# Performance work log

Measured on AMD Instinct MI355X. Metric: run time of the kernel, lower is better.

Reference implementation:

```python
import jax, jax.numpy as jnp
import numpy as np

B, E, WIN, DX, DZ, RAW = 2048, 32, 10, 14, 14, 22

def _leaky(x):
    return jnp.where(x >= 0, x, 0.01 * x)

def setup_inputs():
    key = jax.random.key(0)
    ks = jax.random.split(key, 20)
    def w(k, i, o):
        return jax.random.normal(k, (i, o), dtype=jnp.float32) / np.float32(np.sqrt(i))
    def b(k, o):
        return jax.random.normal(k, (o,), dtype=jnp.float32) * 0.01
    return {
        "raw_obs": jax.random.normal(ks[0], (B, WIN, 1, RAW), dtype=jnp.float32),
        "state_prev": jax.random.normal(ks[1], (B, E, WIN, DX), dtype=jnp.float32),
        "pm_w1": w(ks[2], WIN * DX, 256), "pm_b1": b(ks[3], 256),
        "pm_w3": w(ks[4], 256, 512), "pm_b3": b(ks[5], 512),
        "pm_wm2": w(ks[6], 512, DX), "pm_bm2": b(ks[7], DX),
        "sm_w2": w(ks[8], WIN * RAW, 256), "sm_b2": b(ks[9], 256),
        "sm_w3": w(ks[10], 256, 256), "sm_b3": b(ks[11], 256),
        "sm_w5": w(ks[12], 256, 64), "sm_b5": b(ks[13], 64),
        "sm_w6": w(ks[14], 64, DZ), "sm_b6": b(ks[15], DZ),
        "on_w1": w(ks[16], DZ, 32), "on_b1": b(ks[17], 32),
        "on_w2": w(ks[18], 32, DZ), "on_b2": b(ks[19], DZ),
    }

def reference(raw_obs, state_prev, pm_w1, pm_b1, pm_w3, pm_b3, pm_wm2, pm_bm2,
              sm_w2, sm_b2, sm_w3, sm_b3, sm_w5, sm_b5, sm_w6, sm_b6,
              on_w1, on_b1, on_w2, on_b2):
    bs, ens, win, dx = state_prev.shape
    dz = sm_w6.shape[1]
    # --- process model (LinearFlipout evaluated at mean weights) ---
    x = state_prev.reshape(bs * ens, win * dx)
    x = _leaky(x @ pm_w1 + pm_b1)
    x = _leaky(x @ pm_w3 + pm_b3)
    state_pred = (x @ pm_wm2 + pm_bm2).reshape(bs, ens, dx)   # [B,E,dx]
    state_m = state_pred.mean(axis=1)                          # [B,dx]
    A = state_pred - state_m[:, None, :]                       # [B,E,dx]
    # --- sensor model: torch repeat(E,1,1,1) tiles ensemble-major, the final
    # reshape reinterprets as batch-major; replicate that layout faithfully ---
    s = jnp.tile(raw_obs, (ens, 1, 1, 1)).reshape(bs * ens, win * raw_obs.shape[-1])
    s = _leaky(s @ sm_w2 + sm_b2)
    s = _leaky(s @ sm_w3 + sm_b3)
    s = _leaky(s @ sm_w5 + sm_b5)
    s = s @ sm_w6 + sm_b6
    ensemble_z = s.reshape(bs, ens, dz)                        # [B,E,dz]
    z = ensemble_z.mean(axis=1, keepdims=True)                 # [B,1,dz]
    # --- observation noise R = diag_embed(square(mlp(z)+c) + init) ---
    r = jax.nn.relu(z @ on_w1 + on_b1) @ on_w2 + on_b2
    r = jnp.square(r + 0.001) + 0.038729833
    R = r.reshape(bs, dz)[:, :, None] * jnp.eye(dz, dtype=r.dtype)  # [B,dz,dz]
    # --- EnKF correction ---
    S = jnp.einsum('bei,bej->bij', A, A)                       # AT @ A, [B,dx,dx]
    innovation = S / (ens - 1) + R
    K = (S / (ens - 1)) @ jnp.linalg.inv(innovation)           # [B,dx,dz]
    diff = ensemble_z - state_pred                             # (y - H_XT)^T, [B,E,dz]
    gain = jnp.einsum('bij,bej->bei', K, diff)                 # [B,E,dx]
    state_corrected = state_pred + gain
    return (state_corrected,
            state_corrected.mean(axis=1, keepdims=True),
            state_m[:, None, :],
            z,
            ensemble_z)
```

## Files before the change

kernel.cpp:

```cpp
#include <hip/hip_runtime.h>

typedef unsigned short u16;
typedef __attribute__((ext_vector_type(8))) short short8;
typedef __attribute__((ext_vector_type(4))) float floatx4;

#define MFMA_BF16 __builtin_amdgcn_mfma_f32_16x16x32_bf16

__device__ __forceinline__ u16 f2bf(float f) {
    union { float f; unsigned int i; } v; v.f = f;
    unsigned int u = v.i;
    u += 0x7fffu + ((u >> 16) & 1u);
    return (u16)(u >> 16);
}
__device__ __forceinline__ float leaky(float x) { return x >= 0.f ? x : 0.01f * x; }

#define H1S 264
#define RS 232
#define H3S 72
#define CS 136

#define O1 917504
#define O2 946176
#define O3 974848
#define O4 1003520

#define PW1   0
#define PW3   40960
#define PWM2  172032
#define PSW2  180224
#define PSW3  237568
#define PSW5  303104
#define PSW6  319488
#define PTOTAL 320512
#define WS_NEEDED 641024
#define WS_BIG (641024 + 3670016)

struct PackSeg { const float* W; int K, N, S, base, count; };
struct PackArgs { PackSeg seg[7]; };

__global__ __launch_bounds__(256) void pack_all(PackArgs pa, u16* __restrict__ P) {
    int u = blockIdx.x * 256 + threadIdx.x;
    if (u >= PTOTAL) return;
#pragma unroll
    for (int i = 0; i < 7; i++) {
        if (u >= pa.seg[i].base && u < pa.seg[i].base + pa.seg[i].count) {
            int v = u - pa.seg[i].base;
            int j = v & 7;
            int l = (v >> 3) & 63;
            int ts = v >> 9;
            int s = ts % pa.seg[i].S;
            int t = ts / pa.seg[i].S;
            int k = s * 32 + (l >> 4) * 8 + j;
            int n = t * 16 + (l & 15);
            P[u] = (k < pa.seg[i].K && n < pa.seg[i].N)
                       ? f2bf(pa.seg[i].W[k * pa.seg[i].N + n]) : (u16)0;
            return;
        }
    }
}

__device__ __forceinline__ short8 load_x_frag(const float* __restrict__ X,
                                              int row, int s, int q) {
    const float* p = X + row * 140;
    float4 v0 = {0.f, 0.f, 0.f, 0.f}, v1 = {0.f, 0.f, 0.f, 0.f};
    int col0 = s * 32 + q * 8;
    if (s < 4) {
        v0 = *(const float4*)(p + col0);
        v1 = *(const float4*)(p + col0 + 4);
    } else {
        if (q <= 1) v0 = *(const float4*)(p + col0);
        if (q == 0) v1 = *(const float4*)(p + col0 + 4);
    }
    short8 r;
    r[0] = (short)f2bf(v0.x); r[1] = (short)f2bf(v0.y);
    r[2] = (short)f2bf(v0.z); r[3] = (short)f2bf(v0.w);
    r[4] = (short)f2bf(v1.x); r[5] = (short)f2bf(v1.y);
    r[6] = (short)f2bf(v1.z); r[7] = (short)f2bf(v1.w);
    return r;
}

__global__ __launch_bounds__(256) void merged_mlp(
    const float* __restrict__ Rg, const float* __restrict__ Xg,
    const u16* __restrict__ Pk,
    const float* __restrict__ b1, const float* __restrict__ b3,
    const float* __restrict__ bm2,
    const float* __restrict__ b2, const float* __restrict__ sb3,
    const float* __restrict__ b5, const float* __restrict__ b6,
    float* __restrict__ ez_out,
    float* __restrict__ sp_ws)
{
    __shared__ __align__(16) u16 ldsH[64 * H1S];
    __shared__ __align__(16) u16 ldsC[64 * CS];

    const int tid  = threadIdx.x;
    const int lane = tid & 63;
    const int wave = tid >> 6;
    const int q    = lane >> 4;
    const int n16  = lane & 15;

    if (blockIdx.x < 64) {
        const u16* w2p = Pk + PSW2;
        const u16* w3p = Pk + PSW3;
        const u16* w5p = Pk + PSW5;
        const u16* w6p = Pk + PSW6;
        const int row0 = blockIdx.x * 32;

        for (int idx = tid; idx < 32 * 56; idx += 256) {
            int r = idx / 56, c4 = idx - r * 56;
            float4 v = {0.f, 0.f, 0.f, 0.f};
            if (c4 < 55) v = *(const float4*)&Rg[(row0 + r) * 220 + c4 * 4];
            u16* dst = &ldsH[r * RS + c4 * 4];
            dst[0] = f2bf(v.x); dst[1] = f2bf(v.y); dst[2] = f2bf(v.z); dst[3] = f2bf(v.w);
        }
        __syncthreads();

        {
            floatx4 zero = {0.f, 0.f, 0.f, 0.f};
            floatx4 acc[2][4];
            for (int rt = 0; rt < 2; rt++)
                for (int ct = 0; ct < 4; ct++) acc[rt][ct] = zero;
#pragma unroll
            for (int s = 0; s < 7; s++) {
                short8 a0 = *(const short8*)&ldsH[n16 * RS + s * 32 + q * 8];
                short8 a1 = *(const short8*)&ldsH[(n16 + 16) * RS + s * 32 + q * 8];
#pragma unroll
                for (int ct = 0; ct < 4; ct++) {
                    int t = wave * 4 + ct;
                    short8 bf = *(const short8*)&w2p[((t * 7 + s) * 64 + lane) * 8];
                    acc[0][ct] = MFMA_BF16(a0, bf, acc[0][ct], 0, 0, 0);
                    acc[1][ct] = MFMA_BF16(a1, bf, acc[1][ct], 0, 0, 0);
                }
            }
#pragma unroll
            for (int ct = 0; ct < 4; ct++) {
                int col = (wave * 4 + ct) * 16 + n16;
                float bias = b2[col];
#pragma unroll
                for (int rt = 0; rt < 2; rt++)
#pragma unroll
                    for (int r = 0; r < 4; r++)
                        ldsC[(rt * 16 + q * 4 + r) * H1S + col] = f2bf(leaky(acc[rt][ct][r] + bias));
            }
        }
        __syncthreads();

        {
            floatx4 zero = {0.f, 0.f, 0.f, 0.f};
            floatx4 acc[2][4];
            for (int rt = 0; rt < 2; rt++)
                for (int ct = 0; ct < 4; ct++) acc[rt][ct] = zero;
#pragma unroll
            for (int s = 0; s < 8; s++) {
                short8 a0 = *(const short8*)&ldsC[n16 * H1S + s * 32 + q * 8];
                short8 a1 = *(const short8*)&ldsC[(n16 + 16) * H1S + s * 32 + q * 8];
#pragma unroll
                for (int ct = 0; ct < 4; ct++) {
                    int t = wave * 4 + ct;
                    short8 bf = *(const short8*)&w3p[((t * 8 + s) * 64 + lane) * 8];
                    acc[0][ct] = MFMA_BF16(a0, bf, acc[0][ct], 0, 0, 0);
                    acc[1][ct] = MFMA_BF16(a1, bf, acc[1][ct], 0, 0, 0);
                }
            }
#pragma unroll
            for (int ct = 0; ct < 4; ct++) {
                int col = (wave * 4 + ct) * 16 + n16;
                float bias = sb3[col];
#pragma unroll
                for (int rt = 0; rt < 2; rt++)
#pragma unroll
                    for (int r = 0; r < 4; r++)
                        ldsH[(rt * 16 + q * 4 + r) * H1S + col] = f2bf(leaky(acc[rt][ct][r] + bias));
            }
        }
        __syncthreads();

        {
            floatx4 zero = {0.f, 0.f, 0.f, 0.f};
            floatx4 acc[2] = {zero, zero};
#pragma unroll
            for (int s = 0; s < 8; s++) {
                short8 a0 = *(const short8*)&ldsH[n16 * H1S + s * 32 + q * 8];
                short8 a1 = *(const short8*)&ldsH[(n16 + 16) * H1S + s * 32 + q * 8];
                short8 bf = *(const short8*)&w5p[((wave * 8 + s) * 64 + lane) * 8];
                acc[0] = MFMA_BF16(a0, bf, acc[0], 0, 0, 0);
                acc[1] = MFMA_BF16(a1, bf, acc[1], 0, 0, 0);
            }
            int col = wave * 16 + n16;
            float bias = b5[col];
#pragma unroll
            for (int rt = 0; rt < 2; rt++)
#pragma unroll
                for (int r = 0; r < 4; r++)
                    ldsC[(rt * 16 + q * 4 + r) * H3S + col] = f2bf(leaky(acc[rt][r] + bias));
        }
        __syncthreads();

        if (wave < 2) {
            floatx4 zero = {0.f, 0.f, 0.f, 0.f};
            floatx4 acc[2] = {zero, zero};
            int s = wave;
            short8 a0 = *(const short8*)&ldsC[n16 * H3S + s * 32 + q * 8];
            short8 a1 = *(const short8*)&ldsC[(n16 + 16) * H3S + s * 32 + q * 8];
            short8 bf = *(const short8*)&w6p[(s * 64 + lane) * 8];
            acc[0] = MFMA_BF16(a0, bf, acc[0], 0, 0, 0);
            acc[1] = MFMA_BF16(a1, bf, acc[1], 0, 0, 0);
            float* pacc = (float*)ldsH;
#pragma unroll
            for (int rt = 0; rt < 2; rt++)
#pragma unroll
                for (int r = 0; r < 4; r++)
                    pacc[(wave * 32 + rt * 16 + q * 4 + r) * 16 + n16] = acc[rt][r];
        }
        __syncthreads();
        {
            const float* pacc = (const float*)ldsH;
            for (int idx = tid; idx < 512; idx += 256) {
                int r = idx >> 4, c = idx & 15;
                float v = pacc[idx] + pacc[512 + idx];
                if (c < 14) ez_out[(row0 + r) * 14 + c] = v + b6[c];
            }
        }
    } else {
        const u16* w1p  = Pk + PW1;
        const u16* w3p  = Pk + PW3;
        const u16* wm2p = Pk + PWM2;
        const int bb   = blockIdx.x - 64;
        const int row0 = bb * 64;

        {
            floatx4 zero = {0.f, 0.f, 0.f, 0.f};
            floatx4 acc[4][4];
            for (int rt = 0; rt < 4; rt++)
                for (int ct = 0; ct < 4; ct++) acc[rt][ct] = zero;
#pragma unroll
            for (int s = 0; s < 5; s++) {
                short8 a[4];
#pragma unroll
                for (int rt = 0; rt < 4; rt++)
                    a[rt] = load_x_frag(Xg, row0 + rt * 16 + n16, s, q);
#pragma unroll
                for (int ct = 0; ct < 4; ct++) {
                    int t = wave * 4 + ct;
                    short8 bf = *(const short8*)&w1p[((t * 5 + s) * 64 + lane) * 8];
#pragma unroll
                    for (int rt = 0; rt < 4; rt++)
                        acc[rt][ct] = MFMA_BF16(a[rt], bf, acc[rt][ct], 0, 0, 0);
                }
            }
#pragma unroll
            for (int ct = 0; ct < 4; ct++) {
                int col = (wave * 4 + ct) * 16 + n16;
                float bias = b1[col];
#pragma unroll
                for (int rt = 0; rt < 4; rt++)
#pragma unroll
                    for (int r = 0; r < 4; r++)
                        ldsH[(rt * 16 + q * 4 + r) * H1S + col] = f2bf(leaky(acc[rt][ct][r] + bias));
            }
        }
        __syncthreads();

        floatx4 acc3[4];
        {
            floatx4 zero = {0.f, 0.f, 0.f, 0.f};
            for (int rt = 0; rt < 4; rt++) acc3[rt] = zero;
        }
#pragma unroll
        for (int c = 0; c < 4; c++) {
            {
                floatx4 zero = {0.f, 0.f, 0.f, 0.f};
                floatx4 acc[4][2];
                for (int rt = 0; rt < 4; rt++)
                    for (int ct = 0; ct < 2; ct++) acc[rt][ct] = zero;
#pragma unroll
                for (int s = 0; s < 8; s++) {
                    short8 a[4];
#pragma unroll
                    for (int rt = 0; rt < 4; rt++)
                        a[rt] = *(const short8*)&ldsH[(rt * 16 + n16) * H1S + s * 32 + q * 8];
#pragma unroll
                    for (int ct = 0; ct < 2; ct++) {
                        int tg = c * 8 + wave * 2 + ct;
                        short8 bf = *(const short8*)&w3p[((tg * 8 + s) * 64 + lane) * 8];
#pragma unroll
                        for (int rt = 0; rt < 4; rt++)
                            acc[rt][ct] = MFMA_BF16(a[rt], bf, acc[rt][ct], 0, 0, 0);
                    }
                }
#pragma unroll
                for (int ct = 0; ct < 2; ct++) {
                    int cl = (wave * 2 + ct) * 16 + n16;
                    float bias = b3[c * 128 + cl];
#pragma unroll
                    for (int rt = 0; rt < 4; rt++)
#pragma unroll
                        for (int r = 0; r < 4; r++)
                            ldsC[(rt * 16 + q * 4 + r) * CS + cl] = f2bf(leaky(acc[rt][ct][r] + bias));
                }
            }
            __syncthreads();
            {
                int sg = c * 4 + wave;
                short8 bf = *(const short8*)&wm2p[(sg * 64 + lane) * 8];
#pragma unroll
                for (int rt = 0; rt < 4; rt++) {
                    short8 a = *(const short8*)&ldsC[(rt * 16 + n16) * CS + wave * 32 + q * 8];
                    acc3[rt] = MFMA_BF16(a, bf, acc3[rt], 0, 0, 0);
                }
            }
            __syncthreads();
        }

        {
            float* pacc = (float*)ldsH;
#pragma unroll
            for (int rt = 0; rt < 4; rt++)
#pragma unroll
                for (int r = 0; r < 4; r++)
                    pacc[(wave * 64 + rt * 16 + q * 4 + r) * 16 + n16] = acc3[rt][r];
        }
        __syncthreads();
        {
            const float* pacc = (const float*)ldsH;
            for (int idx = tid; idx < 1024; idx += 256) {
                int r = idx >> 4, c = idx & 15;
                float v = pacc[idx] + pacc[1024 + idx] + pacc[2048 + idx] + pacc[3072 + idx];
                if (c < 14) sp_ws[(row0 + r) * 14 + c] = v + bm2[c];
            }
        }
    }
}

__global__ __launch_bounds__(64) void enkf_tail(
    const float* __restrict__ sp_all,
    const float* __restrict__ on_w1, const float* __restrict__ on_b1,
    const float* __restrict__ on_w2, const float* __restrict__ on_b2,
    float* out)
{
    __shared__ float spv[32][14];
    __shared__ float ezv[32][14];
    __shared__ float smv[14], zzv[14], rrv[14];
    __shared__ float M[14][14], Kmat[14][14];
    __shared__ float G[14][28];
    __shared__ float fac[14];
    __shared__ float hbuf[32];

    const int l = threadIdx.x;
    const int b = blockIdx.x;

    for (int idx = l; idx < 448; idx += 64) ((float*)spv)[idx] = sp_all[b * 448 + idx];
    {
        const float* ezsrc = out + O4 + (b & 63) * 448;
        for (int idx = l; idx < 448; idx += 64) ((float*)ezv)[idx] = ezsrc[idx];
    }

    if (l < 14) {
        float s1 = 0.f, s2 = 0.f;
        for (int e = 0; e < 32; e++) { s1 += spv[e][l]; s2 += ezv[e][l]; }
        smv[l] = s1 * (1.f / 32.f);
        zzv[l] = s2 * (1.f / 32.f);
    }
    if (l < 32) {
        float t = on_b1[l];
        for (int k = 0; k < 14; k++) t += zzv[k] * on_w1[k * 32 + l];
        hbuf[l] = t > 0.f ? t : 0.f;
    }
    if (l < 14) {
        float t = on_b2[l];
        for (int k = 0; k < 32; k++) t += hbuf[k] * on_w2[k * 14 + l];
        t += 0.001f;
        rrv[l] = t * t + 0.038729833f;
    }
    for (int idx = l; idx < 196; idx += 64) {
        int i = idx / 14, j = idx - i * 14;
        float s = 0.f;
        for (int e = 0; e < 32; e++) s += (spv[e][i] - smv[i]) * (spv[e][j] - smv[j]);
        s *= (1.f / 31.f);
        M[i][j] = s;
        G[i][j] = s + (i == j ? rrv[i] : 0.f);
        G[i][14 + j] = (i == j) ? 1.f : 0.f;
    }
    for (int c = 0; c < 14; c++) {
        float pinv = 1.f / G[c][c];
        if (l < 28) G[c][l] *= pinv;
        if (l < 14 && l != c) fac[l] = G[l][c];
        for (int idx = l; idx < 392; idx += 64) {
            int i = idx / 28, j = idx - i * 28;
            if (i != c) G[i][j] -= fac[i] * G[c][j];
        }
    }
    for (int idx = l; idx < 196; idx += 64) {
        int i = idx / 14, j = idx - i * 14;
        float s = 0.f;
        for (int k = 0; k < 14; k++) s += M[i][k] * G[k][14 + j];
        Kmat[i][j] = s;
    }
    for (int idx = l; idx < 448; idx += 64) {
        int e = idx / 14, i = idx - e * 14;
        float g = 0.f;
        for (int j = 0; j < 14; j++) g += Kmat[i][j] * (ezv[e][j] - spv[e][j]);
        out[b * 448 + idx] = spv[e][i] + g;
        out[O4 + b * 448 + idx] = ezv[e][i];
    }
    if (l < 14) {
        float g = 0.f;
        for (int j = 0; j < 14; j++) g += Kmat[l][j] * (zzv[j] - smv[j]);
        out[O1 + b * 14 + l] = smv[l] + g;
        out[O2 + b * 14 + l] = smv[l];
        out[O3 + b * 14 + l] = zzv[l];
    }
}

extern "C" void kernel_launch(void* const* d_in, const int* in_sizes, int n_in,
                              void* d_out, int out_size, void* d_ws, size_t ws_size,
                              hipStream_t stream) {
    (void)in_sizes; (void)n_in; (void)out_size; (void)ws_size;

    const float* raw_obs    = (const float*)d_in[0];
    const float* state_prev = (const float*)d_in[1];
    const float* pm_w1  = (const float*)d_in[2];
    const float* pm_b1  = (const float*)d_in[3];
    const float* pm_w3  = (const float*)d_in[4];
    const float* pm_b3  = (const float*)d_in[5];
    const float* pm_wm2 = (const float*)d_in[6];
    const float* pm_bm2 = (const float*)d_in[7];
    const float* sm_w2  = (const float*)d_in[8];
    const float* sm_b2  = (const float*)d_in[9];
    const float* sm_w3  = (const float*)d_in[10];
    const float* sm_b3  = (const float*)d_in[11];
    const float* sm_w5  = (const float*)d_in[12];
    const float* sm_b5  = (const float*)d_in[13];
    const float* sm_w6  = (const float*)d_in[14];
    const float* sm_b6  = (const float*)d_in[15];
    const float* on_w1  = (const float*)d_in[16];
    const float* on_b1  = (const float*)d_in[17];
    const float* on_w2  = (const float*)d_in[18];
    const float* on_b2  = (const float*)d_in[19];

    float* out = (float*)d_out;
    u16* P = (u16*)d_ws;
    float* sp_ws = (float*)((char*)d_ws + WS_NEEDED);

    PackArgs pa;
    pa.seg[0] = { pm_w1,  140, 256, 5,  PW1,  40960  };
    pa.seg[1] = { pm_w3,  256, 512, 8,  PW3,  131072 };
    pa.seg[2] = { pm_wm2, 512, 14,  16, PWM2, 8192   };
    pa.seg[3] = { sm_w2,  220, 256, 7,  PSW2, 57344  };
    pa.seg[4] = { sm_w3,  256, 256, 8,  PSW3, 65536  };
    pa.seg[5] = { sm_w5,  256, 64,  8,  PSW5, 16384  };
    pa.seg[6] = { sm_w6,  64,  14,  2,  PSW6, 1024   };
    pack_all<<<(PTOTAL + 255) / 256, 256, 0, stream>>>(pa, P);

    merged_mlp<<<1088, 256, 0, stream>>>(raw_obs, state_prev, P,
                                         pm_b1, pm_b3, pm_bm2,
                                         sm_b2, sm_b3, sm_b5, sm_b6,
                                         out + O4, sp_ws);
    enkf_tail<<<2048, 64, 0, stream>>>(sp_ws, on_w1, on_b1, on_w2, on_b2, out);
}
```

Baseline: 190.3 us.

## Halve process-model row tile and shrink LDS to raise occupancy

Result: faster. 183.1 us (median of 2 runs) (-3.8%).

```diff
diff --git a/kernel.cpp b/kernel.cpp
--- a/kernel.cpp
+++ b/kernel.cpp
@@ -79,7 +79,7 @@
     return r;
 }
 
-__global__ __launch_bounds__(256) void merged_mlp(
+__global__ __launch_bounds__(256, 5) void merged_mlp(
     const float* __restrict__ Rg, const float* __restrict__ Xg,
     const u16* __restrict__ Pk,
     const float* __restrict__ b1, const float* __restrict__ b3,
@@ -89,8 +89,8 @@
     float* __restrict__ ez_out,
     float* __restrict__ sp_ws)
 {
-    __shared__ __align__(16) u16 ldsH[64 * H1S];
-    __shared__ __align__(16) u16 ldsC[64 * CS];
+    __shared__ __align__(16) u16 ldsH[32 * H1S];
+    __shared__ __align__(16) u16 ldsC[32 * CS];
 
     const int tid  = threadIdx.x;
     const int lane = tid & 63;
@@ -114,11 +114,11 @@
         }
         __syncthreads();
 
-        {
-            floatx4 zero = {0.f, 0.f, 0.f, 0.f};
-            floatx4 acc[2][4];
-            for (int rt = 0; rt < 2; rt++)
-                for (int ct = 0; ct < 4; ct++) acc[rt][ct] = zero;
+        floatx4 acc1[2][4];
+        {
+            floatx4 zero = {0.f, 0.f, 0.f, 0.f};
+            for (int rt = 0; rt < 2; rt++)
+                for (int ct = 0; ct < 4; ct++) acc1[rt][ct] = zero;
 #pragma unroll
             for (int s = 0; s < 7; s++) {
                 short8 a0 = *(const short8*)&ldsH[n16 * RS + s * 32 + q * 8];
@@ -127,71 +127,79 @@
                 for (int ct = 0; ct < 4; ct++) {
                     int t = wave * 4 + ct;
                     short8 bf = *(const short8*)&w2p[((t * 7 + s) * 64 + lane) * 8];
-                    acc[0][ct] = MFMA_BF16(a0, bf, acc[0][ct], 0, 0, 0);
-                    acc[1][ct] = MFMA_BF16(a1, bf, acc[1][ct], 0, 0, 0);
-                }
-            }
-#pragma unroll
-            for (int ct = 0; ct < 4; ct++) {
-                int col = (wave * 4 + ct) * 16 + n16;
-                float bias = b2[col];
-#pragma unroll
-                for (int rt = 0; rt < 2; rt++)
-#pragma unroll
-                    for (int r = 0; r < 4; r++)
-                        ldsC[(rt * 16 + q * 4 + r) * H1S + col] = f2bf(leaky(acc[rt][ct][r] + bias));
-            }
-        }
-        __syncthreads();
-
-        {
-            floatx4 zero = {0.f, 0.f, 0.f, 0.f};
-            floatx4 acc[2][4];
-            for (int rt = 0; rt < 2; rt++)
-                for (int ct = 0; ct < 4; ct++) acc[rt][ct] = zero;
-#pragma unroll
-            for (int s = 0; s < 8; s++) {
-                short8 a0 = *(const short8*)&ldsC[n16 * H1S + s * 32 + q * 8];
-                short8 a1 = *(const short8*)&ldsC[(n16 + 16) * H1S + s * 32 + q * 8];
-#pragma unroll
-                for (int ct = 0; ct < 4; ct++) {
-                    int t = wave * 4 + ct;
-                    short8 bf = *(const short8*)&w3p[((t * 8 + s) * 64 + lane) * 8];
-                    acc[0][ct] = MFMA_BF16(a0, bf, acc[0][ct], 0, 0, 0);
-                    acc[1][ct] = MFMA_BF16(a1, bf, acc[1][ct], 0, 0, 0);
-                }
-            }
-#pragma unroll
-            for (int ct = 0; ct < 4; ct++) {
-                int col = (wave * 4 + ct) * 16 + n16;
-                float bias = sb3[col];
-#pragma unroll
-                for (int rt = 0; rt < 2; rt++)
-#pragma unroll
-                    for (int r = 0; r < 4; r++)
-                        ldsH[(rt * 16 + q * 4 + r) * H1S + col] = f2bf(leaky(acc[rt][ct][r] + bias));
-            }
-        }
-        __syncthreads();
-
-        {
-            floatx4 zero = {0.f, 0.f, 0.f, 0.f};
-            floatx4 acc[2] = {zero, zero};
+                    acc1[0][ct] = MFMA_BF16(a0, bf, acc1[0][ct], 0, 0, 0);
+                    acc1[1][ct] = MFMA_BF16(a1, bf, acc1[1][ct], 0, 0, 0);
+                }
+            }
+        }
+        __syncthreads();
+#pragma unroll
+        for (int ct = 0; ct < 4; ct++) {
+            int col = (wave * 4 + ct) * 16 + n16;
+            float bias = b2[col];
+#pragma unroll
+            for (int rt = 0; rt < 2; rt++)
+#pragma unroll
+                for (int r = 0; r < 4; r++)
+                    ldsH[(rt * 16 + q * 4 + r) * H1S + col] = f2bf(leaky(acc1[rt][ct][r] + bias));
+        }
+        __syncthreads();
+
+        floatx4 acc5[2];
+        {
+            floatx4 zero = {0.f, 0.f, 0.f, 0.f};
+            acc5[0] = zero; acc5[1] = zero;
+        }
+#pragma unroll
+        for (int c = 0; c < 2; c++) {
+            floatx4 zero = {0.f, 0.f, 0.f, 0.f};
+            floatx4 acc[2][2];
+            for (int rt = 0; rt < 2; rt++)
+                for (int ct = 0; ct < 2; ct++) acc[rt][ct] = zero;
 #pragma unroll
             for (int s = 0; s < 8; s++) {
                 short8 a0 = *(const short8*)&ldsH[n16 * H1S + s * 32 + q * 8];
                 short8 a1 = *(const short8*)&ldsH[(n16 + 16) * H1S + s * 32 + q * 8];
-                short8 bf = *(const short8*)&w5p[((wave * 8 + s) * 64 + lane) * 8];
-                acc[0] = MFMA_BF16(a0, bf, acc[0], 0, 0, 0);
-                acc[1] = MFMA_BF16(a1, bf, acc[1], 0, 0, 0);
-            }
+#pragma unroll
+                for (int ct = 0; ct < 2; ct++) {
+                    int tg = c * 8 + wave * 2 + ct;
+                    short8 bf = *(const short8*)&w3p[((tg * 8 + s) * 64 + lane) * 8];
+                    acc[0][ct] = MFMA_BF16(a0, bf, acc[0][ct], 0, 0, 0);
+                    acc[1][ct] = MFMA_BF16(a1, bf, acc[1][ct], 0, 0, 0);
+                }
+            }
+#pragma unroll
+            for (int ct = 0; ct < 2; ct++) {
+                int cl = (wave * 2 + ct) * 16 + n16;
+                float bias = sb3[c * 128 + cl];
+#pragma unroll
+                for (int rt = 0; rt < 2; rt++)
+#pragma unroll
+                    for (int r = 0; r < 4; r++)
+                        ldsC[(rt * 16 + q * 4 + r) * CS + cl] = f2bf(leaky(acc[rt][ct][r] + bias));
+            }
+            __syncthreads();
+#pragma unroll
+            for (int sl = 0; sl < 4; sl++) {
+                int sg = c * 4 + sl;
+                short8 bf = *(const short8*)&w5p[((wave * 8 + sg) * 64 + lane) * 8];
+#pragma unroll
+                for (int rt = 0; rt < 2; rt++) {
+                    short8 a = *(const short8*)&ldsC[(rt * 16 + n16) * CS + sl * 32 + q * 8];
+                    acc5[rt] = MFMA_BF16(a, bf, acc5[rt], 0, 0, 0);
+                }
+            }
+            __syncthreads();
+        }
+
+        {
             int col = wave * 16 + n16;
             float bias = b5[col];
 #pragma unroll
             for (int rt = 0; rt < 2; rt++)
 #pragma unroll
                 for (int r = 0; r < 4; r++)
-                    ldsC[(rt * 16 + q * 4 + r) * H3S + col] = f2bf(leaky(acc[rt][r] + bias));
+                    ldsC[(rt * 16 + q * 4 + r) * H3S + col] = f2bf(leaky(acc5[rt][r] + bias));
         }
         __syncthreads();
 
@@ -225,26 +233,23 @@
         const u16* w3p  = Pk + PW3;
         const u16* wm2p = Pk + PWM2;
         const int bb   = blockIdx.x - 64;
-        const int row0 = bb * 64;
-
-        {
-            floatx4 zero = {0.f, 0.f, 0.f, 0.f};
-            floatx4 acc[4][4];
-            for (int rt = 0; rt < 4; rt++)
+        const int row0 = bb * 32;
+
+        {
+            floatx4 zero = {0.f, 0.f, 0.f, 0.f};
+            floatx4 acc[2][4];
+            for (int rt = 0; rt < 2; rt++)
                 for (int ct = 0; ct < 4; ct++) acc[rt][ct] = zero;
 #pragma unroll
             for (int s = 0; s < 5; s++) {
-                short8 a[4];
-#pragma unroll
-                for (int rt = 0; rt < 4; rt++)
-                    a[rt] = load_x_frag(Xg, row0 + rt * 16 + n16, s, q);
+                short8 a0 = load_x_frag(Xg, row0 + n16, s, q);
+                short8 a1 = load_x_frag(Xg, row0 + 16 + n16, s, q);
 #pragma unroll
                 for (int ct = 0; ct < 4; ct++) {
                     int t = wave * 4 + ct;
                     short8 bf = *(const short8*)&w1p[((t * 5 + s) * 64 + lane) * 8];
-#pragma unroll
-                    for (int rt = 0; rt < 4; rt++)
-                        acc[rt][ct] = MFMA_BF16(a[rt], bf, acc[rt][ct], 0, 0, 0);
+                    acc[0][ct] = MFMA_BF16(a0, bf, acc[0][ct], 0, 0, 0);
+                    acc[1][ct] = MFMA_BF16(a1, bf, acc[1][ct], 0, 0, 0);
                 }
             }
 #pragma unroll
@@ -252,7 +257,7 @@
                 int col = (wave * 4 + ct) * 16 + n16;
                 float bias = b1[col];
 #pragma unroll
-                for (int rt = 0; rt < 4; rt++)
+                for (int rt = 0; rt < 2; rt++)
 #pragma unroll
                     for (int r = 0; r < 4; r++)
                         ldsH[(rt * 16 + q * 4 + r) * H1S + col] = f2bf(leaky(acc[rt][ct][r] + bias));
@@ -260,50 +265,45 @@
         }
         __syncthreads();
 
-        floatx4 acc3[4];
-        {
-            floatx4 zero = {0.f, 0.f, 0.f, 0.f};
-            for (int rt = 0; rt < 4; rt++) acc3[rt] = zero;
+        floatx4 acc3[2];
+        {
+            floatx4 zero = {0.f, 0.f, 0.f, 0.f};
+            acc3[0] = zero; acc3[1] = zero;
         }
 #pragma unroll
         for (int c = 0; c < 4; c++) {
-            {
-                floatx4 zero = {0.f, 0.f, 0.f, 0.f};
-                floatx4 acc[4][2];
-                for (int rt = 0; rt < 4; rt++)
-                    for (int ct = 0; ct < 2; ct++) acc[rt][ct] = zero;
-#pragma unroll
-                for (int s = 0; s < 8; s++) {
-                    short8 a[4];
-#pragma unroll
-                    for (int rt = 0; rt < 4; rt++)
-                        a[rt] = *(const short8*)&ldsH[(rt * 16 + n16) * H1S + s * 32 + q * 8];
-#pragma unroll
-                    for (int ct = 0; ct < 2; ct++) {
-                        int tg = c * 8 + wave * 2 + ct;
-                        short8 bf = *(const short8*)&w3p[((tg * 8 + s) * 64 + lane) * 8];
-#pragma unroll
-                        for (int rt = 0; rt < 4; rt++)
-                            acc[rt][ct] = MFMA_BF16(a[rt], bf, acc[rt][ct], 0, 0, 0);
-                    }
-                }
+            floatx4 zero = {0.f, 0.f, 0.f, 0.f};
+            floatx4 acc[2][2];
+            for (int rt = 0; rt < 2; rt++)
+                for (int ct = 0; ct < 2; ct++) acc[rt][ct] = zero;
+#pragma unroll
+            for (int s = 0; s < 8; s++) {
+                short8 a0 = *(const short8*)&ldsH[n16 * H1S + s * 32 + q * 8];
+                short8 a1 = *(const short8*)&ldsH[(n16 + 16) * H1S + s * 32 + q * 8];
 #pragma unroll
                 for (int ct = 0; ct < 2; ct++) {
-                    int cl = (wave * 2 + ct) * 16 + n16;
-                    float bias = b3[c * 128 + cl];
-#pragma unroll
-                    for (int rt = 0; rt < 4; rt++)
-#pragma unroll
-                        for (int r = 0; r < 4; r++)
-                            ldsC[(rt * 16 + q * 4 + r) * CS + cl] = f2bf(leaky(acc[rt][ct][r] + bias));
-                }
+                    int tg = c * 8 + wave * 2 + ct;
+                    short8 bf = *(const short8*)&w3p[((tg * 8 + s) * 64 + lane) * 8];
+                    acc[0][ct] = MFMA_BF16(a0, bf, acc[0][ct], 0, 0, 0);
+                    acc[1][ct] = MFMA_BF16(a1, bf, acc[1][ct], 0, 0, 0);
+                }
+            }
+#pragma unroll
+            for (int ct = 0; ct < 2; ct++) {
+                int cl = (wave * 2 + ct) * 16 + n16;
+                float bias = b3[c * 128 + cl];
+#pragma unroll
+                for (int rt = 0; rt < 2; rt++)
+#pragma unroll
+                    for (int r = 0; r < 4; r++)
+                        ldsC[(rt * 16 + q * 4 + r) * CS + cl] = f2bf(leaky(acc[rt][ct][r] + bias));
             }
             __syncthreads();
             {
                 int sg = c * 4 + wave;
                 short8 bf = *(const short8*)&wm2p[(sg * 64 + lane) * 8];
 #pragma unroll
-                for (int rt = 0; rt < 4; rt++) {
+                for (int rt = 0; rt < 2; rt++) {
                     short8 a = *(const short8*)&ldsC[(rt * 16 + n16) * CS + wave * 32 + q * 8];
                     acc3[rt] = MFMA_BF16(a, bf, acc3[rt], 0, 0, 0);
                 }
@@ -314,17 +314,17 @@
         {
             float* pacc = (float*)ldsH;
 #pragma unroll
-            for (int rt = 0; rt < 4; rt++)
+            for (int rt = 0; rt < 2; rt++)
 #pragma unroll
                 for (int r = 0; r < 4; r++)
-                    pacc[(wave * 64 + rt * 16 + q * 4 + r) * 16 + n16] = acc3[rt][r];
+                    pacc[(wave * 32 + rt * 16 + q * 4 + r) * 16 + n16] = acc3[rt][r];
         }
         __syncthreads();
         {
             const float* pacc = (const float*)ldsH;
-            for (int idx = tid; idx < 1024; idx += 256) {
+            for (int idx = tid; idx < 512; idx += 256) {
                 int r = idx >> 4, c = idx & 15;
-                float v = pacc[idx] + pacc[1024 + idx] + pacc[2048 + idx] + pacc[3072 + idx];
+                float v = pacc[idx] + pacc[512 + idx] + pacc[1024 + idx] + pacc[1536 + idx];
                 if (c < 14) sp_ws[(row0 + r) * 14 + c] = v + bm2[c];
             }
         }
@@ -451,7 +451,7 @@
     pa.seg[6] = { sm_w6,  64,  14,  2,  PSW6, 1024   };
     pack_all<<<(PTOTAL + 255) / 256, 256, 0, stream>>>(pa, P);
 
-    merged_mlp<<<1088, 256, 0, stream>>>(raw_obs, state_prev, P,
+    merged_mlp<<<2112, 256, 0, stream>>>(raw_obs, state_prev, P,
                                          pm_b1, pm_b3, pm_bm2,
                                          sm_b2, sm_b3, sm_b5, sm_b6,
                                          out + O4, sp_ws);
```
